# Optimization experiments

Hardware: AMD Instinct MI355X
Metric: run time of the kernel (lower is better)

The kernel has to match this reference:

```python
import jax, jax.numpy as jnp
import numpy as np

EPS = 1e-12  # matches torch F.normalize default eps
TEMP = 0.1


def _gram(x):
    # L2-normalize rows; for unit vectors 1 - 0.5*||xi-xj||^2 == xi . xj
    n = x / jnp.maximum(jnp.linalg.norm(x, axis=-1, keepdims=True), EPS)
    return n @ n.T  # [N, N]


def setup_inputs() -> dict:
    key = jax.random.key(0)
    k1, k2, k3, k4 = jax.random.split(key, 4)
    N, D = 4096, 512
    return {
        "fm_rgb": jax.random.normal(k1, (N, D), dtype=jnp.float32),
        "fm_depth": jax.random.normal(k2, (N, D), dtype=jnp.float32),
        "fm_ir": jax.random.normal(k3, (N, D), dtype=jnp.float32),
        "fm_t": jax.random.normal(k4, (N, D), dtype=jnp.float32),
    }


def reference(fm_rgb, fm_depth, fm_ir, fm_t):
    G_rgb = _gram(fm_rgb)
    G_depth = _gram(fm_depth)
    G_ir = _gram(fm_ir)
    G_t = _gram(fm_t)
    inv_t = 1.0 / TEMP
    loss_rgb = jnp.mean((G_t * inv_t - G_rgb * inv_t) ** 2)
    loss_depth = jnp.mean((G_t * inv_t - G_depth * inv_t) ** 2)
    loss_ir = jnp.mean((G_t * inv_t - G_ir * inv_t) ** 2)
    return loss_rgb + loss_depth + loss_ir
```

## Files before the change

### kernel.cpp

```cpp
#include <hip/hip_runtime.h>
#include <hip/hip_bf16.h>


typedef __attribute__((ext_vector_type(4))) float floatx4;
typedef __attribute__((ext_vector_type(2))) long long llx2;
typedef __attribute__((ext_vector_type(8))) int intx8;

typedef __attribute__((address_space(3))) unsigned char* lds_u8p;
typedef const __attribute__((address_space(3))) unsigned char* lds_cu8p;

#define N_ROWS 4096
#define DDIM   512
#define LOSS_SCALE 9.094947017729282e-11f

__device__ __forceinline__ const float* sel_mod(int mod, const float* a,
                                                const float* b, const float* c,
                                                const float* d) {
  return mod == 0 ? a : mod == 1 ? b : mod == 2 ? c : d;
}

__device__ __forceinline__ float bfr(float x) {
  __hip_bfloat16 h = __float2bfloat16(x);
  unsigned short u = *(unsigned short*)&h;
  return __uint_as_float(((unsigned int)u) << 16);
}

__device__ __forceinline__ llx2 ldsr16(lds_cu8p p) {
  llx2 r;
  asm volatile("ds_read_b128 %0, %1" : "=v"(r) : "v"(p));
  return r;
}

__global__ __launch_bounds__(512) void preprocess_kernel(
    const float* __restrict__ in0, const float* __restrict__ in1,
    const float* __restrict__ in2, const float* __restrict__ in3,
    unsigned char* __restrict__ nT8, float* __restrict__ out) {
  int mod = blockIdx.y;
  int k0 = blockIdx.x * 64;
  const float* X = sel_mod(mod, in0, in1, in2, in3) + (size_t)k0 * DDIM;

  if (blockIdx.x == 0 && blockIdx.y == 0 && threadIdx.x == 0)
    out[0] = 0.f;

  __shared__ float rsc[64];
  __shared__ unsigned int t8[512 * 17];

  int t = threadIdx.x;
  int a = t >> 5;
  int bg = t & 31;

  float4 v[4][4];
#pragma unroll
  for (int q = 0; q < 4; ++q)
#pragma unroll
    for (int p = 0; p < 4; ++p)
      v[q][p] = ((const float4*)(X + (size_t)(4 * a + q) * DDIM + p * 128))[bg];

  float ss[4];
#pragma unroll
  for (int q = 0; q < 4; ++q) {
    float acc = 0.f;
#pragma unroll
    for (int p = 0; p < 4; ++p) {
      float4 u = v[q][p];
      acc += u.x * u.x + u.y * u.y + u.z * u.z + u.w * u.w;
    }
    ss[q] = acc;
  }
#pragma unroll
  for (int off = 16; off > 0; off >>= 1)
#pragma unroll
    for (int q = 0; q < 4; ++q) ss[q] += __shfl_down(ss[q], off, 32);
  if (bg == 0) {
#pragma unroll
    for (int q = 0; q < 4; ++q)
      rsc[4 * a + q] = 16.0f / fmaxf(sqrtf(ss[q]), 1e-12f);
  }
  __syncthreads();

  float sc[4];
#pragma unroll
  for (int q = 0; q < 4; ++q) sc[q] = rsc[4 * a + q];

#pragma unroll
  for (int p = 0; p < 4; ++p)
#pragma unroll
    for (int j = 0; j < 4; ++j) {
      float f0 = bfr(((const float*)&v[0][p])[j] * sc[0]);
      float f1 = bfr(((const float*)&v[1][p])[j] * sc[1]);
      float f2 = bfr(((const float*)&v[2][p])[j] * sc[2]);
      float f3 = bfr(((const float*)&v[3][p])[j] * sc[3]);
      unsigned int pk = __builtin_amdgcn_cvt_pk_fp8_f32(f0, f1, 0, 0);
      pk = __builtin_amdgcn_cvt_pk_fp8_f32(f2, f3, pk, 1);
      t8[(p * 128 + bg * 4 + j) * 17 + a] = pk;
    }
  __syncthreads();

  size_t rbase = (size_t)(mod * 64 + blockIdx.x) * 32768;
#pragma unroll
  for (int it = 0; it < 4; ++it) {
    int idx = it * 512 + t;
    int col = idx >> 2;
    int g = idx & 3;
    uint4 o;
    o.x = t8[col * 17 + g * 4 + 0];
    o.y = t8[col * 17 + g * 4 + 1];
    o.z = t8[col * 17 + g * 4 + 2];
    o.w = t8[col * 17 + g * 4 + 3];
    *(uint4*)(nT8 + rbase + (size_t)idx * 16) = o;
  }
}

__device__ __forceinline__ void stage_half(
    const unsigned char* __restrict__ mbase, int cbase, int k0,
    lds_u8p dst, int lane) {
  int rr = lane >> 3;
  int s = lane & 7;
  int kb0 = k0 >> 6;
#pragma unroll
  for (int c = 0; c < 8; ++c) {
    int row = c * 8 + rr;
    int gc = s ^ ((row >> 1) & 7);
    const unsigned char* g =
        mbase + ((size_t)(kb0 + (gc >> 2)) * 512 + cbase + row) * 64 +
        (gc & 3) * 16;
    __builtin_amdgcn_global_load_lds(
        (__attribute__((address_space(1))) void*)(void*)g,
        (__attribute__((address_space(3))) void*)(dst + c * 1024),
        16, 0, 0);
  }
}

__device__ __forceinline__ void compute_w(lds_cu8p lsb, floatx4 acc[4][2],
                                          int wn, int lm, int lq) {
  intx8 A8[4], B8[2];
#pragma unroll
  for (int mi = 0; mi < 4; ++mi) {
    int row = mi * 16 + lm;
    int sw = (row >> 1) & 7;
    *(llx2*)&A8[mi] = ldsr16(lsb + row * 128 + ((lq * 2) ^ sw) * 16);
    *((llx2*)&A8[mi] + 1) =
        ldsr16(lsb + row * 128 + ((lq * 2 + 1) ^ sw) * 16);
  }
#pragma unroll
  for (int ni = 0; ni < 2; ++ni) {
    int row = wn + ni * 16 + lm;
    int sw = (row >> 1) & 7;
    *(llx2*)&B8[ni] =
        ldsr16(lsb + 8192 + row * 128 + ((lq * 2) ^ sw) * 16);
    *((llx2*)&B8[ni] + 1) =
        ldsr16(lsb + 8192 + row * 128 + ((lq * 2 + 1) ^ sw) * 16);
  }
  asm volatile("s_waitcnt lgkmcnt(0)");
  __builtin_amdgcn_sched_barrier(0);
  __builtin_amdgcn_s_setprio(1);
#pragma unroll
  for (int mi = 0; mi < 4; ++mi)
#pragma unroll
    for (int ni = 0; ni < 2; ++ni)
      acc[mi][ni] = __builtin_amdgcn_mfma_scale_f32_16x16x128_f8f6f4(
          A8[mi], B8[ni], acc[mi][ni], 0, 0,
          0, 0x7F, 0, 0x7F);
  __builtin_amdgcn_s_setprio(0);
}

__global__ __launch_bounds__(128) void gram_frob_kernel(
    const unsigned char* __restrict__ nT8, float* __restrict__ out) {
  __shared__ __align__(16) unsigned char ls[5][16384];

  int bx = blockIdx.x;
  int job = (bx & 7) * 42 + (bx >> 3);

  int rem = job, ti = 7, tj = 7;
  for (int i = 0; i < 8; ++i) {
    int rowlen = 7 + 10 * (7 - i);
    if (rem < rowlen) {
      if (rem < 7) {
        ti = i; tj = i;
      } else {
        int r2 = rem - 7;
        ti = i; tj = i + 1 + r2 / 10;
        rem = r2 % 10;
      }
      break;
    }
    rem -= rowlen;
  }

  int pa_, pb_, a0, b0;
  float wgt;
  if (ti == tj) {
    if (rem < 4) { pa_ = pb_ = rem; wgt = (rem == 3) ? 3.f : 1.f; }
    else         { pa_ = 3; pb_ = rem - 4; wgt = -2.f; }
    a0 = ti * 64; b0 = ti * 64;
  } else {
    if (rem < 4) {
      pa_ = pb_ = rem; wgt = (rem == 3) ? 6.f : 2.f;
      a0 = ti * 64; b0 = tj * 64;
    } else {
      int k = rem - 4;
      pa_ = 3; pb_ = k >> 1; wgt = -2.f;
      if (k & 1) { a0 = tj * 64; b0 = ti * 64; }
      else       { a0 = ti * 64; b0 = tj * 64; }
    }
  }

  const unsigned char* Abase = nT8 + (size_t)pa_ * 2097152;
  const unsigned char* Bbase = nT8 + (size_t)pb_ * 2097152;

  int t = threadIdx.x;
  int w = t >> 6;
  int lane = t & 63;
  int lm = lane & 15;
  int lq = lane >> 4;
  int wn = w * 32;
  const unsigned char* mbase = (w == 0) ? Abase : Bbase;
  int cb = (w == 0) ? a0 : b0;
  int soff = w * 8192;

  floatx4 zero = {0.f, 0.f, 0.f, 0.f};
  floatx4 acc[4][2];
#pragma unroll
  for (int mi = 0; mi < 4; ++mi)
#pragma unroll
    for (int ni = 0; ni < 2; ++ni) acc[mi][ni] = zero;

  lds_u8p lbase = (lds_u8p)(void*)&ls[0][0];
  lds_u8p p0 = lbase + 0 * 16384 + soff;
  lds_u8p p1 = lbase + 1 * 16384 + soff;
  lds_u8p p2 = lbase + 2 * 16384 + soff;
  lds_u8p p3 = lbase + 3 * 16384 + soff;
  lds_u8p p4 = lbase + 4 * 16384 + soff;
  stage_half(mbase, cb, 0, p0, lane);
  stage_half(mbase, cb, 128, p1, lane);
  stage_half(mbase, cb, 256, p2, lane);
  stage_half(mbase, cb, 384, p3, lane);
  for (int i = 0; i < 28; ++i) {
    asm volatile("s_waitcnt vmcnt(24)");
    __builtin_amdgcn_sched_barrier(0);
    __builtin_amdgcn_s_barrier();
    stage_half(mbase, cb, (i + 4) * 128, p4, lane);
    compute_w((lds_cu8p)(p0 - soff), acc, wn, lm, lq);
    lds_u8p tmp = p0; p0 = p1; p1 = p2; p2 = p3; p3 = p4; p4 = tmp;
  }
  asm volatile("s_waitcnt vmcnt(24)");
  __builtin_amdgcn_sched_barrier(0);
  __builtin_amdgcn_s_barrier();
  compute_w((lds_cu8p)(p0 - soff), acc, wn, lm, lq);
  asm volatile("s_waitcnt vmcnt(16)");
  __builtin_amdgcn_sched_barrier(0);
  __builtin_amdgcn_s_barrier();
  compute_w((lds_cu8p)(p1 - soff), acc, wn, lm, lq);
  asm volatile("s_waitcnt vmcnt(8)");
  __builtin_amdgcn_sched_barrier(0);
  __builtin_amdgcn_s_barrier();
  compute_w((lds_cu8p)(p2 - soff), acc, wn, lm, lq);
  asm volatile("s_waitcnt vmcnt(0)");
  __builtin_amdgcn_sched_barrier(0);
  __builtin_amdgcn_s_barrier();
  compute_w((lds_cu8p)(p3 - soff), acc, wn, lm, lq);

  float s = 0.f;
#pragma unroll
  for (int mi = 0; mi < 4; ++mi)
#pragma unroll
    for (int ni = 0; ni < 2; ++ni)
#pragma unroll
      for (int r = 0; r < 4; ++r) {
        float v = acc[mi][ni][r];
        s += v * v;
      }
#pragma unroll
  for (int off = 32; off > 0; off >>= 1) s += __shfl_down(s, off, 64);
  if (lane == 0)
    atomicAdd(out, wgt * LOSS_SCALE * s);
}

extern "C" void kernel_launch(void* const* d_in, const int* in_sizes, int n_in,
                              void* d_out, int out_size, void* d_ws, size_t ws_size,
                              hipStream_t stream) {
  const float* in_rgb   = (const float*)d_in[0];
  const float* in_depth = (const float*)d_in[1];
  const float* in_ir    = (const float*)d_in[2];
  const float* in_t     = (const float*)d_in[3];

  unsigned char* nT8 = (unsigned char*)d_ws;

  preprocess_kernel<<<dim3(64, 4), 512, 0, stream>>>(
      in_rgb, in_depth, in_ir, in_t, nT8, (float*)d_out);
  gram_frob_kernel<<<dim3(336), 128, 0, stream>>>(nT8, (float*)d_out);
}
```

Before: 101.7 us.

## Split gram tile work across four waves with 2x2 quadrant MFMA layout

The gram kernel grows from two waves to four per block. Each wave now stages a quarter of the A/B tiles and computes a 32x32 quadrant of the 64x64 output tile, where before each wave did half. The waitcnt thresholds change to match the smaller per-wave load count, and per-wave partial sums are combined in shared memory before one atomic per block. This is meant to double the waves available to hide latency on a grid of only 336 blocks, at the cost of an extra block-wide sync and more LDS reads per MFMA.

```diff
diff --git a/kernel.cpp b/kernel.cpp
--- a/kernel.cpp
+++ b/kernel.cpp
@@ -111,15 +111,15 @@
   }
 }
 
-__device__ __forceinline__ void stage_half(
+__device__ __forceinline__ void stage_q(
     const unsigned char* __restrict__ mbase, int cbase, int k0,
-    lds_u8p dst, int lane) {
+    lds_u8p dst, int lane, int rowoff) {
   int rr = lane >> 3;
   int s = lane & 7;
   int kb0 = k0 >> 6;
 #pragma unroll
-  for (int c = 0; c < 8; ++c) {
-    int row = c * 8 + rr;
+  for (int c = 0; c < 4; ++c) {
+    int row = rowoff + c * 8 + rr;
     int gc = s ^ ((row >> 1) & 7);
     const unsigned char* g =
         mbase + ((size_t)(kb0 + (gc >> 2)) * 512 + cbase + row) * 64 +
@@ -131,12 +131,12 @@
   }
 }
 
-__device__ __forceinline__ void compute_w(lds_cu8p lsb, floatx4 acc[4][2],
-                                          int wn, int lm, int lq) {
-  intx8 A8[4], B8[2];
-#pragma unroll
-  for (int mi = 0; mi < 4; ++mi) {
-    int row = mi * 16 + lm;
+__device__ __forceinline__ void compute_q(lds_cu8p lsb, floatx4 acc[2][2],
+                                          int mh, int nh, int lm, int lq) {
+  intx8 A8[2], B8[2];
+#pragma unroll
+  for (int mi = 0; mi < 2; ++mi) {
+    int row = 32 * mh + mi * 16 + lm;
     int sw = (row >> 1) & 7;
     *(llx2*)&A8[mi] = ldsr16(lsb + row * 128 + ((lq * 2) ^ sw) * 16);
     *((llx2*)&A8[mi] + 1) =
@@ -144,7 +144,7 @@
   }
 #pragma unroll
   for (int ni = 0; ni < 2; ++ni) {
-    int row = wn + ni * 16 + lm;
+    int row = 32 * nh + ni * 16 + lm;
     int sw = (row >> 1) & 7;
     *(llx2*)&B8[ni] =
         ldsr16(lsb + 8192 + row * 128 + ((lq * 2) ^ sw) * 16);
@@ -155,7 +155,7 @@
   __builtin_amdgcn_sched_barrier(0);
   __builtin_amdgcn_s_setprio(1);
 #pragma unroll
-  for (int mi = 0; mi < 4; ++mi)
+  for (int mi = 0; mi < 2; ++mi)
 #pragma unroll
     for (int ni = 0; ni < 2; ++ni)
       acc[mi][ni] = __builtin_amdgcn_mfma_scale_f32_16x16x128_f8f6f4(
@@ -164,9 +164,10 @@
   __builtin_amdgcn_s_setprio(0);
 }
 
-__global__ __launch_bounds__(128) void gram_frob_kernel(
+__global__ __launch_bounds__(256) void gram_frob_kernel(
     const unsigned char* __restrict__ nT8, float* __restrict__ out) {
   __shared__ __align__(16) unsigned char ls[5][16384];
+  __shared__ float red[4];
 
   int bx = blockIdx.x;
   int job = (bx & 7) * 42 + (bx >> 3);
@@ -213,56 +214,55 @@
   int lane = t & 63;
   int lm = lane & 15;
   int lq = lane >> 4;
-  int wn = w * 32;
-  const unsigned char* mbase = (w == 0) ? Abase : Bbase;
-  int cb = (w == 0) ? a0 : b0;
-  int soff = w * 8192;
+  int mh = w >> 1;
+  int nh = w & 1;
+  const unsigned char* mbase = (w < 2) ? Abase : Bbase;
+  int cbase = (w < 2) ? a0 : b0;
+  int rowoff = (w & 1) * 32;
+  int dsoff = (w >= 2 ? 8192 : 0) + (w & 1) * 4096;
 
   floatx4 zero = {0.f, 0.f, 0.f, 0.f};
-  floatx4 acc[4][2];
-#pragma unroll
-  for (int mi = 0; mi < 4; ++mi)
-#pragma unroll
-    for (int ni = 0; ni < 2; ++ni) acc[mi][ni] = zero;
+  floatx4 acc[2][2];
+  acc[0][0] = zero; acc[0][1] = zero; acc[1][0] = zero; acc[1][1] = zero;
 
   lds_u8p lbase = (lds_u8p)(void*)&ls[0][0];
-  lds_u8p p0 = lbase + 0 * 16384 + soff;
-  lds_u8p p1 = lbase + 1 * 16384 + soff;
-  lds_u8p p2 = lbase + 2 * 16384 + soff;
-  lds_u8p p3 = lbase + 3 * 16384 + soff;
-  lds_u8p p4 = lbase + 4 * 16384 + soff;
-  stage_half(mbase, cb, 0, p0, lane);
-  stage_half(mbase, cb, 128, p1, lane);
-  stage_half(mbase, cb, 256, p2, lane);
-  stage_half(mbase, cb, 384, p3, lane);
+  lds_u8p p0 = lbase + 0 * 16384 + dsoff;
+  lds_u8p p1 = lbase + 1 * 16384 + dsoff;
+  lds_u8p p2 = lbase + 2 * 16384 + dsoff;
+  lds_u8p p3 = lbase + 3 * 16384 + dsoff;
+  lds_u8p p4 = lbase + 4 * 16384 + dsoff;
+  stage_q(mbase, cbase, 0, p0, lane, rowoff);
+  stage_q(mbase, cbase, 128, p1, lane, rowoff);
+  stage_q(mbase, cbase, 256, p2, lane, rowoff);
+  stage_q(mbase, cbase, 384, p3, lane, rowoff);
   for (int i = 0; i < 28; ++i) {
-    asm volatile("s_waitcnt vmcnt(24)");
+    asm volatile("s_waitcnt vmcnt(12)");
     __builtin_amdgcn_sched_barrier(0);
     __builtin_amdgcn_s_barrier();
-    stage_half(mbase, cb, (i + 4) * 128, p4, lane);
-    compute_w((lds_cu8p)(p0 - soff), acc, wn, lm, lq);
+    stage_q(mbase, cbase, (i + 4) * 128, p4, lane, rowoff);
+    compute_q((lds_cu8p)(p0 - dsoff), acc, mh, nh, lm, lq);
     lds_u8p tmp = p0; p0 = p1; p1 = p2; p2 = p3; p3 = p4; p4 = tmp;
   }
-  asm volatile("s_waitcnt vmcnt(24)");
-  __builtin_amdgcn_sched_barrier(0);
-  __builtin_amdgcn_s_barrier();
-  compute_w((lds_cu8p)(p0 - soff), acc, wn, lm, lq);
-  asm volatile("s_waitcnt vmcnt(16)");
-  __builtin_amdgcn_sched_barrier(0);
-  __builtin_amdgcn_s_barrier();
-  compute_w((lds_cu8p)(p1 - soff), acc, wn, lm, lq);
+  asm volatile("s_waitcnt vmcnt(12)");
+  __builtin_amdgcn_sched_barrier(0);
+  __builtin_amdgcn_s_barrier();
+  compute_q((lds_cu8p)(p0 - dsoff), acc, mh, nh, lm, lq);
   asm volatile("s_waitcnt vmcnt(8)");
   __builtin_amdgcn_sched_barrier(0);
   __builtin_amdgcn_s_barrier();
-  compute_w((lds_cu8p)(p2 - soff), acc, wn, lm, lq);
+  compute_q((lds_cu8p)(p1 - dsoff), acc, mh, nh, lm, lq);
+  asm volatile("s_waitcnt vmcnt(4)");
+  __builtin_amdgcn_sched_barrier(0);
+  __builtin_amdgcn_s_barrier();
+  compute_q((lds_cu8p)(p2 - dsoff), acc, mh, nh, lm, lq);
   asm volatile("s_waitcnt vmcnt(0)");
   __builtin_amdgcn_sched_barrier(0);
   __builtin_amdgcn_s_barrier();
-  compute_w((lds_cu8p)(p3 - soff), acc, wn, lm, lq);
+  compute_q((lds_cu8p)(p3 - dsoff), acc, mh, nh, lm, lq);
 
   float s = 0.f;
 #pragma unroll
-  for (int mi = 0; mi < 4; ++mi)
+  for (int mi = 0; mi < 2; ++mi)
 #pragma unroll
     for (int ni = 0; ni < 2; ++ni)
 #pragma unroll
@@ -272,8 +272,12 @@
       }
 #pragma unroll
   for (int off = 32; off > 0; off >>= 1) s += __shfl_down(s, off, 64);
-  if (lane == 0)
-    atomicAdd(out, wgt * LOSS_SCALE * s);
+  if (lane == 0) red[w] = s;
+  __syncthreads();
+  if (t == 0) {
+    float tot = red[0] + red[1] + red[2] + red[3];
+    atomicAdd(out, wgt * LOSS_SCALE * tot);
+  }
 }
 
 extern "C" void kernel_launch(void* const* d_in, const int* in_sizes, int n_in,
@@ -288,5 +292,5 @@
 
   preprocess_kernel<<<dim3(64, 4), 512, 0, stream>>>(
       in_rgb, in_depth, in_ir, in_t, nT8, (float*)d_out);
-  gram_frob_kernel<<<dim3(336), 128, 0, stream>>>(nT8, (float*)d_out);
-}
+  gram_frob_kernel<<<dim3(336), 256, 0, stream>>>(nT8, (float*)d_out);
+}
```

Measured after the change: 103.9 us. 1.02x slower.

## Fuse preprocess and gram kernels into one cooperative launch with grid sync

Applied to the files above, without the earlier changes.

Merges the normalize/quantize preprocessing and the FP8 gram Frobenius kernel into a single cooperative kernel of 256 blocks of 512 threads, with a grid-wide sync between the phases. Each block then runs up to two 128-thread gram sub-jobs in separate LDS regions, and the pipeline drops from 5 to 4 stages to fit. The goal is to remove the second kernel launch and the gap between kernels. In exchange it adds grid-sync cost, leaves half of each block's threads idle in the compute phase, and lets some blocks' work be imbalanced (slots 256 and above are doubled up).

```diff
diff --git a/kernel.cpp b/kernel.cpp
--- a/kernel.cpp
+++ b/kernel.cpp
@@ -1,5 +1,8 @@
 #include <hip/hip_runtime.h>
 #include <hip/hip_bf16.h>
+#include <hip/hip_cooperative_groups.h>
+
+namespace cg = cooperative_groups;
 
 
 typedef __attribute__((ext_vector_type(4))) float floatx4;
@@ -29,86 +32,6 @@
   llx2 r;
   asm volatile("ds_read_b128 %0, %1" : "=v"(r) : "v"(p));
   return r;
-}
-
-__global__ __launch_bounds__(512) void preprocess_kernel(
-    const float* __restrict__ in0, const float* __restrict__ in1,
-    const float* __restrict__ in2, const float* __restrict__ in3,
-    unsigned char* __restrict__ nT8, float* __restrict__ out) {
-  int mod = blockIdx.y;
-  int k0 = blockIdx.x * 64;
-  const float* X = sel_mod(mod, in0, in1, in2, in3) + (size_t)k0 * DDIM;
-
-  if (blockIdx.x == 0 && blockIdx.y == 0 && threadIdx.x == 0)
-    out[0] = 0.f;
-
-  __shared__ float rsc[64];
-  __shared__ unsigned int t8[512 * 17];
-
-  int t = threadIdx.x;
-  int a = t >> 5;
-  int bg = t & 31;
-
-  float4 v[4][4];
-#pragma unroll
-  for (int q = 0; q < 4; ++q)
-#pragma unroll
-    for (int p = 0; p < 4; ++p)
-      v[q][p] = ((const float4*)(X + (size_t)(4 * a + q) * DDIM + p * 128))[bg];
-
-  float ss[4];
-#pragma unroll
-  for (int q = 0; q < 4; ++q) {
-    float acc = 0.f;
-#pragma unroll
-    for (int p = 0; p < 4; ++p) {
-      float4 u = v[q][p];
-      acc += u.x * u.x + u.y * u.y + u.z * u.z + u.w * u.w;
-    }
-    ss[q] = acc;
-  }
-#pragma unroll
-  for (int off = 16; off > 0; off >>= 1)
-#pragma unroll
-    for (int q = 0; q < 4; ++q) ss[q] += __shfl_down(ss[q], off, 32);
-  if (bg == 0) {
-#pragma unroll
-    for (int q = 0; q < 4; ++q)
-      rsc[4 * a + q] = 16.0f / fmaxf(sqrtf(ss[q]), 1e-12f);
-  }
-  __syncthreads();
-
-  float sc[4];
-#pragma unroll
-  for (int q = 0; q < 4; ++q) sc[q] = rsc[4 * a + q];
-
-#pragma unroll
-  for (int p = 0; p < 4; ++p)
-#pragma unroll
-    for (int j = 0; j < 4; ++j) {
-      float f0 = bfr(((const float*)&v[0][p])[j] * sc[0]);
-      float f1 = bfr(((const float*)&v[1][p])[j] * sc[1]);
-      float f2 = bfr(((const float*)&v[2][p])[j] * sc[2]);
-      float f3 = bfr(((const float*)&v[3][p])[j] * sc[3]);
-      unsigned int pk = __builtin_amdgcn_cvt_pk_fp8_f32(f0, f1, 0, 0);
-      pk = __builtin_amdgcn_cvt_pk_fp8_f32(f2, f3, pk, 1);
-      t8[(p * 128 + bg * 4 + j) * 17 + a] = pk;
-    }
-  __syncthreads();
-
-  size_t rbase = (size_t)(mod * 64 + blockIdx.x) * 32768;
-#pragma unroll
-  for (int it = 0; it < 4; ++it) {
-    int idx = it * 512 + t;
-    int col = idx >> 2;
-    int g = idx & 3;
-    uint4 o;
-    o.x = t8[col * 17 + g * 4 + 0];
-    o.y = t8[col * 17 + g * 4 + 1];
-    o.z = t8[col * 17 + g * 4 + 2];
-    o.w = t8[col * 17 + g * 4 + 3];
-    *(uint4*)(nT8 + rbase + (size_t)idx * 16) = o;
-  }
 }
 
 __device__ __forceinline__ void stage_half(
@@ -164,116 +87,199 @@
   __builtin_amdgcn_s_setprio(0);
 }
 
-__global__ __launch_bounds__(128) void gram_frob_kernel(
-    const unsigned char* __restrict__ nT8, float* __restrict__ out) {
-  __shared__ __align__(16) unsigned char ls[5][16384];
+__global__ __launch_bounds__(512) void fused_kernel(
+    const float* __restrict__ in0, const float* __restrict__ in1,
+    const float* __restrict__ in2, const float* __restrict__ in3,
+    unsigned char* __restrict__ nT8, float* __restrict__ out) {
+  __shared__ __align__(16) unsigned char smem[131072];
+  __shared__ float red[8];
 
   int bx = blockIdx.x;
-  int job = (bx & 7) * 42 + (bx >> 3);
-
-  int rem = job, ti = 7, tj = 7;
-  for (int i = 0; i < 8; ++i) {
-    int rowlen = 7 + 10 * (7 - i);
-    if (rem < rowlen) {
-      if (rem < 7) {
-        ti = i; tj = i;
-      } else {
-        int r2 = rem - 7;
-        ti = i; tj = i + 1 + r2 / 10;
-        rem = r2 % 10;
+  int t = threadIdx.x;
+
+  {
+    int mod = bx >> 6;
+    int k0 = (bx & 63) * 64;
+    const float* X = sel_mod(mod, in0, in1, in2, in3) + (size_t)k0 * DDIM;
+
+    if (bx == 0 && t == 0) out[0] = 0.f;
+
+    float* rsc = (float*)smem;
+    unsigned int* t8 = (unsigned int*)(smem + 256);
+
+    int a = t >> 5;
+    int bg = t & 31;
+
+    float4 v[4][4];
+#pragma unroll
+    for (int q = 0; q < 4; ++q)
+#pragma unroll
+      for (int p = 0; p < 4; ++p)
+        v[q][p] =
+            ((const float4*)(X + (size_t)(4 * a + q) * DDIM + p * 128))[bg];
+
+    float ss[4];
+#pragma unroll
+    for (int q = 0; q < 4; ++q) {
+      float acc = 0.f;
+#pragma unroll
+      for (int p = 0; p < 4; ++p) {
+        float4 u = v[q][p];
+        acc += u.x * u.x + u.y * u.y + u.z * u.z + u.w * u.w;
       }
-      break;
-    }
-    rem -= rowlen;
-  }
-
-  int pa_, pb_, a0, b0;
-  float wgt;
-  if (ti == tj) {
-    if (rem < 4) { pa_ = pb_ = rem; wgt = (rem == 3) ? 3.f : 1.f; }
-    else         { pa_ = 3; pb_ = rem - 4; wgt = -2.f; }
-    a0 = ti * 64; b0 = ti * 64;
-  } else {
-    if (rem < 4) {
-      pa_ = pb_ = rem; wgt = (rem == 3) ? 6.f : 2.f;
-      a0 = ti * 64; b0 = tj * 64;
-    } else {
-      int k = rem - 4;
-      pa_ = 3; pb_ = k >> 1; wgt = -2.f;
-      if (k & 1) { a0 = tj * 64; b0 = ti * 64; }
-      else       { a0 = ti * 64; b0 = tj * 64; }
-    }
-  }
-
-  const unsigned char* Abase = nT8 + (size_t)pa_ * 2097152;
-  const unsigned char* Bbase = nT8 + (size_t)pb_ * 2097152;
-
-  int t = threadIdx.x;
-  int w = t >> 6;
-  int lane = t & 63;
+      ss[q] = acc;
+    }
+#pragma unroll
+    for (int off = 16; off > 0; off >>= 1)
+#pragma unroll
+      for (int q = 0; q < 4; ++q) ss[q] += __shfl_down(ss[q], off, 32);
+    if (bg == 0) {
+#pragma unroll
+      for (int q = 0; q < 4; ++q)
+        rsc[4 * a + q] = 16.0f / fmaxf(sqrtf(ss[q]), 1e-12f);
+    }
+    __syncthreads();
+
+    float sc[4];
+#pragma unroll
+    for (int q = 0; q < 4; ++q) sc[q] = rsc[4 * a + q];
+
+#pragma unroll
+    for (int p = 0; p < 4; ++p)
+#pragma unroll
+      for (int j = 0; j < 4; ++j) {
+        float f0 = bfr(((const float*)&v[0][p])[j] * sc[0]);
+        float f1 = bfr(((const float*)&v[1][p])[j] * sc[1]);
+        float f2 = bfr(((const float*)&v[2][p])[j] * sc[2]);
+        float f3 = bfr(((const float*)&v[3][p])[j] * sc[3]);
+        unsigned int pk = __builtin_amdgcn_cvt_pk_fp8_f32(f0, f1, 0, 0);
+        pk = __builtin_amdgcn_cvt_pk_fp8_f32(f2, f3, pk, 1);
+        t8[(p * 128 + bg * 4 + j) * 17 + a] = pk;
+      }
+    __syncthreads();
+
+    size_t rbase = (size_t)(mod * 64 + (bx & 63)) * 32768;
+#pragma unroll
+    for (int it = 0; it < 4; ++it) {
+      int idx = it * 512 + t;
+      int col = idx >> 2;
+      int g = idx & 3;
+      uint4 o;
+      o.x = t8[col * 17 + g * 4 + 0];
+      o.y = t8[col * 17 + g * 4 + 1];
+      o.z = t8[col * 17 + g * 4 + 2];
+      o.w = t8[col * 17 + g * 4 + 3];
+      *(uint4*)(nT8 + rbase + (size_t)idx * 16) = o;
+    }
+  }
+
+  cg::this_grid().sync();
+
+  int sub = t >> 7;
+  int tl = t & 127;
+  int slot = bx + 256 * sub;
+  bool active = (sub < 2) && (slot < 336);
+
+  float wgt = 0.f;
+  int w = tl >> 6;
+  int lane = tl & 63;
   int lm = lane & 15;
   int lq = lane >> 4;
   int wn = w * 32;
-  const unsigned char* mbase = (w == 0) ? Abase : Bbase;
-  int cb = (w == 0) ? a0 : b0;
-  int soff = w * 8192;
-
-  floatx4 zero = {0.f, 0.f, 0.f, 0.f};
-  floatx4 acc[4][2];
-#pragma unroll
-  for (int mi = 0; mi < 4; ++mi)
-#pragma unroll
-    for (int ni = 0; ni < 2; ++ni) acc[mi][ni] = zero;
-
-  lds_u8p lbase = (lds_u8p)(void*)&ls[0][0];
-  lds_u8p p0 = lbase + 0 * 16384 + soff;
-  lds_u8p p1 = lbase + 1 * 16384 + soff;
-  lds_u8p p2 = lbase + 2 * 16384 + soff;
-  lds_u8p p3 = lbase + 3 * 16384 + soff;
-  lds_u8p p4 = lbase + 4 * 16384 + soff;
-  stage_half(mbase, cb, 0, p0, lane);
-  stage_half(mbase, cb, 128, p1, lane);
-  stage_half(mbase, cb, 256, p2, lane);
-  stage_half(mbase, cb, 384, p3, lane);
-  for (int i = 0; i < 28; ++i) {
-    asm volatile("s_waitcnt vmcnt(24)");
+
+  if (active) {
+    int job = (slot & 7) * 42 + (slot >> 3);
+
+    int rem = job, ti = 7, tj = 7;
+    for (int i = 0; i < 8; ++i) {
+      int rowlen = 7 + 10 * (7 - i);
+      if (rem < rowlen) {
+        if (rem < 7) {
+          ti = i; tj = i;
+        } else {
+          int r2 = rem - 7;
+          ti = i; tj = i + 1 + r2 / 10;
+          rem = r2 % 10;
+        }
+        break;
+      }
+      rem -= rowlen;
+    }
+
+    int pa_, pb_, a0, b0;
+    if (ti == tj) {
+      if (rem < 4) { pa_ = pb_ = rem; wgt = (rem == 3) ? 3.f : 1.f; }
+      else         { pa_ = 3; pb_ = rem - 4; wgt = -2.f; }
+      a0 = ti * 64; b0 = ti * 64;
+    } else {
+      if (rem < 4) {
+        pa_ = pb_ = rem; wgt = (rem == 3) ? 6.f : 2.f;
+        a0 = ti * 64; b0 = tj * 64;
+      } else {
+        int k = rem - 4;
+        pa_ = 3; pb_ = k >> 1; wgt = -2.f;
+        if (k & 1) { a0 = tj * 64; b0 = ti * 64; }
+        else       { a0 = ti * 64; b0 = tj * 64; }
+      }
+    }
+
+    const unsigned char* Abase = nT8 + (size_t)pa_ * 2097152;
+    const unsigned char* Bbase = nT8 + (size_t)pb_ * 2097152;
+    const unsigned char* mbase = (w == 0) ? Abase : Bbase;
+    int cb = (w == 0) ? a0 : b0;
+    int soff = w * 8192;
+    lds_u8p sb = (lds_u8p)(void*)&smem[0] + sub * 65536;
+
+    floatx4 zero = {0.f, 0.f, 0.f, 0.f};
+    floatx4 acc[4][2];
+#pragma unroll
+    for (int mi = 0; mi < 4; ++mi)
+#pragma unroll
+      for (int ni = 0; ni < 2; ++ni) acc[mi][ni] = zero;
+
+    stage_half(mbase, cb, 0, sb + 0 * 16384 + soff, lane);
+    stage_half(mbase, cb, 128, sb + 1 * 16384 + soff, lane);
+    stage_half(mbase, cb, 256, sb + 2 * 16384 + soff, lane);
+    for (int i = 0; i < 29; ++i) {
+      asm volatile("s_waitcnt vmcnt(16)");
+      __builtin_amdgcn_sched_barrier(0);
+      __builtin_amdgcn_s_barrier();
+      stage_half(mbase, cb, (i + 3) * 128,
+                 sb + ((i + 3) & 3) * 16384 + soff, lane);
+      compute_w((lds_cu8p)(sb + (i & 3) * 16384), acc, wn, lm, lq);
+    }
+    asm volatile("s_waitcnt vmcnt(16)");
     __builtin_amdgcn_sched_barrier(0);
     __builtin_amdgcn_s_barrier();
-    stage_half(mbase, cb, (i + 4) * 128, p4, lane);
-    compute_w((lds_cu8p)(p0 - soff), acc, wn, lm, lq);
-    lds_u8p tmp = p0; p0 = p1; p1 = p2; p2 = p3; p3 = p4; p4 = tmp;
-  }
-  asm volatile("s_waitcnt vmcnt(24)");
-  __builtin_amdgcn_sched_barrier(0);
-  __builtin_amdgcn_s_barrier();
-  compute_w((lds_cu8p)(p0 - soff), acc, wn, lm, lq);
-  asm volatile("s_waitcnt vmcnt(16)");
-  __builtin_amdgcn_sched_barrier(0);
-  __builtin_amdgcn_s_barrier();
-  compute_w((lds_cu8p)(p1 - soff), acc, wn, lm, lq);
-  asm volatile("s_waitcnt vmcnt(8)");
-  __builtin_amdgcn_sched_barrier(0);
-  __builtin_amdgcn_s_barrier();
-  compute_w((lds_cu8p)(p2 - soff), acc, wn, lm, lq);
-  asm volatile("s_waitcnt vmcnt(0)");
-  __builtin_amdgcn_sched_barrier(0);
-  __builtin_amdgcn_s_barrier();
-  compute_w((lds_cu8p)(p3 - soff), acc, wn, lm, lq);
-
-  float s = 0.f;
-#pragma unroll
-  for (int mi = 0; mi < 4; ++mi)
-#pragma unroll
-    for (int ni = 0; ni < 2; ++ni)
-#pragma unroll
-      for (int r = 0; r < 4; ++r) {
-        float v = acc[mi][ni][r];
-        s += v * v;
-      }
-#pragma unroll
-  for (int off = 32; off > 0; off >>= 1) s += __shfl_down(s, off, 64);
-  if (lane == 0)
-    atomicAdd(out, wgt * LOSS_SCALE * s);
+    compute_w((lds_cu8p)(sb + 1 * 16384), acc, wn, lm, lq);
+    asm volatile("s_waitcnt vmcnt(8)");
+    __builtin_amdgcn_sched_barrier(0);
+    __builtin_amdgcn_s_barrier();
+    compute_w((lds_cu8p)(sb + 2 * 16384), acc, wn, lm, lq);
+    asm volatile("s_waitcnt vmcnt(0)");
+    __builtin_amdgcn_sched_barrier(0);
+    __builtin_amdgcn_s_barrier();
+    compute_w((lds_cu8p)(sb + 3 * 16384), acc, wn, lm, lq);
+
+    float s = 0.f;
+#pragma unroll
+    for (int mi = 0; mi < 4; ++mi)
+#pragma unroll
+      for (int ni = 0; ni < 2; ++ni)
+#pragma unroll
+        for (int r = 0; r < 4; ++r) {
+          float v = acc[mi][ni][r];
+          s += v * v;
+        }
+#pragma unroll
+    for (int off = 32; off > 0; off >>= 1) s += __shfl_down(s, off, 64);
+    if (lane == 0) red[(sub << 1) | w] = s;
+  } else {
+    for (int i = 0; i < 32; ++i) __builtin_amdgcn_s_barrier();
+  }
+  __syncthreads();
+  if (active && tl == 0)
+    atomicAdd(out, wgt * LOSS_SCALE * (red[sub * 2] + red[sub * 2 + 1]));
 }
 
 extern "C" void kernel_launch(void* const* d_in, const int* in_sizes, int n_in,
@@ -283,10 +289,16 @@
   const float* in_depth = (const float*)d_in[1];
   const float* in_ir    = (const float*)d_in[2];
   const float* in_t     = (const float*)d_in[3];
-
   unsigned char* nT8 = (unsigned char*)d_ws;
-
-  preprocess_kernel<<<dim3(64, 4), 512, 0, stream>>>(
-      in_rgb, in_depth, in_ir, in_t, nT8, (float*)d_out);
-  gram_frob_kernel<<<dim3(336), 128, 0, stream>>>(nT8, (float*)d_out);
-}
+  float* outp = (float*)d_out;
+
+  void* args[6];
+  args[0] = (void*)&in_rgb;
+  args[1] = (void*)&in_depth;
+  args[2] = (void*)&in_ir;
+  args[3] = (void*)&in_t;
+  args[4] = (void*)&nT8;
+  args[5] = (void*)&outp;
+  hipLaunchCooperativeKernel((const void*)fused_kernel, dim3(256), dim3(512),
+                             args, 0, stream);
+}
```

New measurement: 151.3 us. +48.7%, slower.
